# Performance work log

Measured on AMD Instinct MI355X. Metric: run time of the kernel, lower is better.

## Reference

```python
import jax, jax.numpy as jnp
import numpy as np

D_MODEL = 1024
NHEAD = 16
D_HEAD = D_MODEL // NHEAD
B, L = 2, 2048


def setup_inputs() -> dict:
    key = jax.random.key(0)
    ks = jax.random.split(key, 11)
    s = 1.0 / np.sqrt(D_MODEL)
    return {
        "Q": jax.random.normal(ks[0], (B, L, D_MODEL), jnp.float32),
        "K": jax.random.normal(ks[1], (B, L, D_MODEL), jnp.float32),
        "V": jax.random.normal(ks[2], (B, L, D_MODEL), jnp.float32),
        "Wq": jax.random.normal(ks[3], (D_MODEL, D_MODEL), jnp.float32) * s,
        "bq": jax.random.normal(ks[4], (D_MODEL,), jnp.float32) * 0.01,
        "Wk": jax.random.normal(ks[5], (D_MODEL, D_MODEL), jnp.float32) * s,
        "bk": jax.random.normal(ks[6], (D_MODEL,), jnp.float32) * 0.01,
        "Wv": jax.random.normal(ks[7], (D_MODEL, D_MODEL), jnp.float32) * s,
        "bv": jax.random.normal(ks[8], (D_MODEL,), jnp.float32) * 0.01,
        "Wo": jax.random.normal(ks[9], (D_MODEL, D_MODEL), jnp.float32) * s,
        "bo": jax.random.normal(ks[10], (D_MODEL,), jnp.float32) * 0.01,
    }


def reference(Q, K, V, Wq, bq, Wk, bk, Wv, bv, Wo, bo):
    b, l, _ = Q.shape
    # QKV linear projections (nn.Linear: x @ W.T + b), then split into heads
    q = (Q @ Wq.T + bq).reshape(b, l, NHEAD, D_HEAD)
    k = (K @ Wk.T + bk).reshape(b, l, NHEAD, D_HEAD)
    v = (V @ Wv.T + bv).reshape(b, l, NHEAD, D_HEAD)
    # scaled dot-product attention: softmax(QK^T / sqrt(d_head)) V
    scale = jnp.asarray(1.0 / np.sqrt(D_HEAD), q.dtype)
    scores = jnp.einsum("bqhd,bkhd->bhqk", q, k) * scale  # [B,H,L,L]
    attn = jax.nn.softmax(scores, axis=-1)
    out = jnp.einsum("bhqk,bkhd->bqhd", attn, v)  # [B,L,H,Dh]
    out = out.reshape(b, l, D_MODEL)  # concat heads
    return out @ Wo.T + bo
```

## Files before the change

kernel.cpp:

```cpp
#include <hip/hip_runtime.h>
#include <cstdint>
#include <cstddef>

#define DM 1024
#define NH 16
#define DH 64
#define NB 2
#define SQ 2048
#define MT (NB*SQ)

typedef float  f32x4  __attribute__((ext_vector_type(4)));
typedef float  f32x16 __attribute__((ext_vector_type(16)));
typedef short  s16x8 __attribute__((ext_vector_type(8)));
typedef short  s16x4 __attribute__((ext_vector_type(4)));

__device__ __forceinline__ unsigned short f2bf(float x) {
    unsigned int u = __float_as_uint(x);
    unsigned int lsb = (u >> 16) & 1u;
    u += 0x7fffu + lsb;
    return (unsigned short)(u >> 16);
}

__device__ __forceinline__ void gload16(const void* g, void* l) {
    __builtin_amdgcn_global_load_lds(
        (const __attribute__((address_space(1))) void*)g,
        (__attribute__((address_space(3))) void*)l,
        16, 0, 0);
}

__global__ __launch_bounds__(256) void castk(const float* __restrict__ in,
                                             unsigned short* __restrict__ out, int n) {
    int i = (blockIdx.x * 256 + threadIdx.x) * 4;
    if (i >= n) return;
    float4 a = *reinterpret_cast<const float4*>(in + i);
    s16x4 r;
    r[0] = (short)f2bf(a.x);
    r[1] = (short)f2bf(a.y);
    r[2] = (short)f2bf(a.z);
    r[3] = (short)f2bf(a.w);
    *reinterpret_cast<s16x4*>(out + i) = r;
}

__device__ __forceinline__ void gemm_core(const unsigned short* __restrict__ A,
                                          const unsigned short* __restrict__ Bm,
                                          int m0, int n0, int t,
                                          unsigned short (*As)[64],
                                          unsigned short (*Bs)[64],
                                          f32x4 acc[4][4]) {
    const int lane = t & 63, w = t >> 6;
    const int wm = (w >> 1) * 64, wn = (w & 1) * 64;
    const int lo = lane & 15, hi = lane >> 4;

    for (int k0 = 0; k0 < DM; k0 += 64) {
#pragma unroll
        for (int i = 0; i < 4; i++) {
            int c = i * 256 + t;
            int r = c >> 3, col = (c & 7) * 8;
            gload16(A  + (size_t)(m0 + r) * DM + k0 + col, &As[r][col]);
            gload16(Bm + (size_t)(n0 + r) * DM + k0 + col, &Bs[r][col]);
        }
        asm volatile("s_waitcnt vmcnt(0)" ::: "memory");
        __syncthreads();

#pragma unroll
        for (int kk = 0; kk < 64; kk += 32) {
            s16x8 a[4], b[4];
#pragma unroll
            for (int mi = 0; mi < 4; mi++)
                a[mi] = *reinterpret_cast<const s16x8*>(&As[wm + mi * 16 + lo][kk + hi * 8]);
#pragma unroll
            for (int ni = 0; ni < 4; ni++)
                b[ni] = *reinterpret_cast<const s16x8*>(&Bs[wn + ni * 16 + lo][kk + hi * 8]);
#pragma unroll
            for (int mi = 0; mi < 4; mi++)
#pragma unroll
                for (int ni = 0; ni < 4; ni++)
                    acc[mi][ni] = __builtin_amdgcn_mfma_f32_16x16x32_bf16(
                        a[mi], b[ni], acc[mi][ni], 0, 0, 0);
        }
        __syncthreads();
    }
}

__global__ __launch_bounds__(256, 3) void gemm_qkv(
    const unsigned short* __restrict__ Qb, const unsigned short* __restrict__ Kb,
    const unsigned short* __restrict__ Vb,
    const unsigned short* __restrict__ Wq, const unsigned short* __restrict__ Wk,
    const unsigned short* __restrict__ Wv,
    const float* __restrict__ bq, const float* __restrict__ bk, const float* __restrict__ bv,
    unsigned short* __restrict__ qp, unsigned short* __restrict__ kp,
    unsigned short* __restrict__ vt) {
    __shared__ __align__(16) unsigned short As[128][64];
    __shared__ __align__(16) unsigned short Bs[128][64];
    const int t = threadIdx.x;
    const int z = blockIdx.z;
    const unsigned short* A    = (z == 0) ? Qb : (z == 1) ? Kb : Vb;
    const unsigned short* Bm   = (z == 0) ? Wq : (z == 1) ? Wk : Wv;
    const float*          bias = (z == 0) ? bq : (z == 1) ? bk : bv;
    const int m0 = blockIdx.y * 128, n0 = blockIdx.x * 128;

    f32x4 acc[4][4] = {};
    gemm_core(A, Bm, m0, n0, t, As, Bs, acc);

    const int lane = t & 63, w = t >> 6;
    const int wm = (w >> 1) * 64, wn = (w & 1) * 64;
    const int lo = lane & 15, hi = lane >> 4;

    if (z < 2) {
        unsigned short* C = z ? kp : qp;
        const float scale = z ? 1.0f : 0.18033688011112042f;
#pragma unroll
        for (int mi = 0; mi < 4; mi++)
#pragma unroll
            for (int ni = 0; ni < 4; ni++) {
                int cc = n0 + wn + ni * 16 + lo;
                float bb = bias[cc];
#pragma unroll
                for (int j = 0; j < 4; j++) {
                    int rr = m0 + wm + mi * 16 + hi * 4 + j;
                    C[(size_t)rr * DM + cc] = f2bf((acc[mi][ni][j] + bb) * scale);
                }
            }
    } else {
#pragma unroll
        for (int mi = 0; mi < 4; mi++)
#pragma unroll
            for (int ni = 0; ni < 4; ni++) {
                int cc = n0 + wn + ni * 16 + lo;
                float bb = bias[cc];
#pragma unroll
                for (int j = 0; j < 4; j++) {
                    int rr = m0 + wm + mi * 16 + hi * 4 + j;
                    size_t idx = ((size_t)(rr >> 11) * DM + cc) * SQ + (rr & (SQ - 1));
                    vt[idx] = f2bf(acc[mi][ni][j] + bb);
                }
            }
    }
}

__global__ __launch_bounds__(256, 3) void gemm_out(
    const unsigned short* __restrict__ Ao, const unsigned short* __restrict__ Wo,
    const float* __restrict__ bo, float* __restrict__ Cout) {
    __shared__ __align__(16) unsigned short As[128][64];
    __shared__ __align__(16) unsigned short Bs[128][64];
    const int t = threadIdx.x;
    const int m0 = blockIdx.y * 128, n0 = blockIdx.x * 128;

    f32x4 acc[4][4] = {};
    gemm_core(Ao, Wo, m0, n0, t, As, Bs, acc);

    const int lane = t & 63, w = t >> 6;
    const int wm = (w >> 1) * 64, wn = (w & 1) * 64;
    const int lo = lane & 15, hi = lane >> 4;
#pragma unroll
    for (int mi = 0; mi < 4; mi++)
#pragma unroll
        for (int ni = 0; ni < 4; ni++) {
            int cc = n0 + wn + ni * 16 + lo;
            float bb = bo[cc];
#pragma unroll
            for (int j = 0; j < 4; j++) {
                int rr = m0 + wm + mi * 16 + hi * 4 + j;
                Cout[(size_t)rr * DM + cc] = acc[mi][ni][j] + bb;
            }
        }
}

__global__ __launch_bounds__(256, 2) void attn_k(
    const unsigned short* __restrict__ qp, const unsigned short* __restrict__ kp,
    const unsigned short* __restrict__ vt, unsigned short* __restrict__ ao) {
    __shared__ __align__(16) unsigned short Qs[128][64];
    __shared__ __align__(16) unsigned short Ks[128][64];
    __shared__ __align__(16) unsigned short Vs[64][128];

    const int t = threadIdx.x;
    const int lane = t & 63, w = t >> 6;
    const int l5 = lane & 31, hb = lane >> 5;
    const int q0 = blockIdx.x * 128;
    const int bh = blockIdx.y;
    const int b = bh >> 4, h = bh & 15;

#pragma unroll
    for (int i = 0; i < 4; i++) {
        int c = i * 256 + t;
        int r = c >> 3, col = ((c & 7) ^ (r & 7)) * 8;
        gload16(qp + (size_t)(b * SQ + q0 + r) * DM + h * DH + col, &Qs[r][(c & 7) * 8]);
    }

    float mrow = -1e30f, lrow = 0.0f;
    f32x16 oaccT[2] = {};
    s16x8 qfrag[4];

    for (int kt = 0; kt < SQ; kt += 128) {
#pragma unroll
        for (int i = 0; i < 4; i++) {
            int c = i * 256 + t;
            int r = c >> 3, col = ((c & 7) ^ (r & 7)) * 8;
            gload16(kp + (size_t)(b * SQ + kt + r) * DM + h * DH + col, &Ks[r][(c & 7) * 8]);
        }
#pragma unroll
        for (int i = 0; i < 4; i++) {
            int c = i * 256 + t;
            int r = c >> 4, col = ((c & 15) ^ (r & 15)) * 8;
            gload16(vt + (size_t)(bh * DH + r) * SQ + kt + col, &Vs[r][(c & 15) * 8]);
        }
        asm volatile("s_waitcnt vmcnt(0)" ::: "memory");
        __syncthreads();

        if (kt == 0) {
#pragma unroll
            for (int kk = 0; kk < 4; kk++) {
                int qr = w * 32 + l5;
                qfrag[kk] = *reinterpret_cast<const s16x8*>(
                    &Qs[qr][((kk * 2 + hb) ^ (qr & 7)) * 8]);
            }
        }

        f32x16 sT[4] = {};
#pragma unroll
        for (int ks = 0; ks < 4; ks++) {
#pragma unroll
            for (int kk = 0; kk < 4; kk++) {
                int kr = ks * 32 + l5;
                s16x8 kf = *reinterpret_cast<const s16x8*>(
                    &Ks[kr][((kk * 2 + hb) ^ (kr & 7)) * 8]);
                sT[ks] = __builtin_amdgcn_mfma_f32_32x32x16_bf16(
                    kf, qfrag[kk], sT[ks], 0, 0, 0);
            }
        }

        float mx = -3.0e38f;
#pragma unroll
        for (int ks = 0; ks < 4; ks++) {
            float a0 = fmaxf(fmaxf(sT[ks][0], sT[ks][1]), fmaxf(sT[ks][2], sT[ks][3]));
            float a1 = fmaxf(fmaxf(sT[ks][4], sT[ks][5]), fmaxf(sT[ks][6], sT[ks][7]));
            float a2 = fmaxf(fmaxf(sT[ks][8], sT[ks][9]), fmaxf(sT[ks][10], sT[ks][11]));
            float a3 = fmaxf(fmaxf(sT[ks][12], sT[ks][13]), fmaxf(sT[ks][14], sT[ks][15]));
            mx = fmaxf(mx, fmaxf(fmaxf(a0, a1), fmaxf(a2, a3)));
        }
        mx = fmaxf(mx, __shfl_xor(mx, 32));
        float mnew = fmaxf(mrow, mx);
        float fs = exp2f(mrow - mnew);
        mrow = mnew;
        float ps = 0.0f;
#pragma unroll
        for (int ks = 0; ks < 4; ks++)
#pragma unroll
            for (int r = 0; r < 16; r++) {
                float e = exp2f(sT[ks][r] - mnew);
                sT[ks][r] = e;
                ps += e;
            }
        ps += __shfl_xor(ps, 32);
        lrow = lrow * fs + ps;
        oaccT[0] *= fs;
        oaccT[1] *= fs;

#pragma unroll
        for (int ks = 0; ks < 4; ks++) {
            unsigned int pw0[4], pw1[4];
#pragma unroll
            for (int m = 0; m < 4; m++) {
                pw0[m] = (unsigned int)f2bf(sT[ks][4 * m]) |
                         ((unsigned int)f2bf(sT[ks][4 * m + 1]) << 16);
                pw1[m] = (unsigned int)f2bf(sT[ks][4 * m + 2]) |
                         ((unsigned int)f2bf(sT[ks][4 * m + 3]) << 16);
            }
#pragma unroll
            for (int tt = 0; tt < 2; tt++) {
                unsigned int s0 = hb ? pw0[2 * tt] : pw0[2 * tt + 1];
                unsigned int s1 = hb ? pw1[2 * tt] : pw1[2 * tt + 1];
                unsigned int r0 = __shfl_xor(s0, 32);
                unsigned int r1 = __shfl_xor(s1, 32);
                union { unsigned int u[4]; s16x8 v; } uu;
                if (hb == 0) { uu.u[0] = pw0[2 * tt]; uu.u[1] = pw1[2 * tt];
                               uu.u[2] = r0;          uu.u[3] = r1; }
                else         { uu.u[0] = r0;          uu.u[1] = r1;
                               uu.u[2] = pw0[2 * tt + 1]; uu.u[3] = pw1[2 * tt + 1]; }
                s16x8 pf = uu.v;
#pragma unroll
                for (int dblk = 0; dblk < 2; dblk++) {
                    int vr = dblk * 32 + l5;
                    int sl = ((ks * 2 + tt) * 2 + hb) ^ (vr & 15);
                    s16x8 vf = *reinterpret_cast<const s16x8*>(&Vs[vr][sl * 8]);
                    oaccT[dblk] = __builtin_amdgcn_mfma_f32_32x32x16_bf16(
                        vf, pf, oaccT[dblk], 0, 0, 0);
                }
            }
        }
        __syncthreads();
    }

    float inv = 1.0f / lrow;
    size_t rowbase = (size_t)(b * SQ + q0 + w * 32 + l5) * DM + h * DH;
#pragma unroll
    for (int dblk = 0; dblk < 2; dblk++)
#pragma unroll
        for (int g = 0; g < 4; g++) {
            s16x4 st;
#pragma unroll
            for (int j = 0; j < 4; j++)
                st[j] = (short)f2bf(oaccT[dblk][4 * g + j] * inv);
            *reinterpret_cast<s16x4*>(&ao[rowbase + dblk * 32 + 8 * g + 4 * hb]) = st;
        }
}

extern "C" void kernel_launch(void* const* d_in, const int* in_sizes, int n_in,
                              void* d_out, int out_size, void* d_ws, size_t ws_size,
                              hipStream_t stream) {
    const float* Q  = (const float*)d_in[0];
    const float* K  = (const float*)d_in[1];
    const float* V  = (const float*)d_in[2];
    const float* Wq = (const float*)d_in[3];
    const float* bq = (const float*)d_in[4];
    const float* Wk = (const float*)d_in[5];
    const float* bk = (const float*)d_in[6];
    const float* Wv = (const float*)d_in[7];
    const float* bv = (const float*)d_in[8];
    const float* Wo = (const float*)d_in[9];
    const float* bo = (const float*)d_in[10];

    char* ws = (char*)d_ws;
    size_t off = 0;
    auto alloc = [&](size_t bytes) {
        void* p = ws + off;
        off += (bytes + 255) & ~(size_t)255;
        return p;
    };
    const size_t XB = (size_t)MT * DM * 2;
    const size_t WB = (size_t)DM * DM * 2;
    unsigned short* qb  = (unsigned short*)alloc(XB);
    unsigned short* kb  = (unsigned short*)alloc(XB);
    unsigned short* vb  = (unsigned short*)alloc(XB);
    unsigned short* wqb = (unsigned short*)alloc(WB);
    unsigned short* wkb = (unsigned short*)alloc(WB);
    unsigned short* wvb = (unsigned short*)alloc(WB);
    unsigned short* wob = (unsigned short*)alloc(WB);
    unsigned short* qp  = (unsigned short*)alloc(XB);
    unsigned short* kp  = (unsigned short*)alloc(XB);
    unsigned short* vtp = (unsigned short*)alloc(XB);
    unsigned short* ao  = (unsigned short*)alloc(XB);

    castk<<<dim3(MT * DM / 1024), 256, 0, stream>>>(Q, qb, MT * DM);
    castk<<<dim3(MT * DM / 1024), 256, 0, stream>>>(K, kb, MT * DM);
    castk<<<dim3(MT * DM / 1024), 256, 0, stream>>>(V, vb, MT * DM);
    castk<<<dim3(DM * DM / 1024), 256, 0, stream>>>(Wq, wqb, DM * DM);
    castk<<<dim3(DM * DM / 1024), 256, 0, stream>>>(Wk, wkb, DM * DM);
    castk<<<dim3(DM * DM / 1024), 256, 0, stream>>>(Wv, wvb, DM * DM);
    castk<<<dim3(DM * DM / 1024), 256, 0, stream>>>(Wo, wob, DM * DM);

    gemm_qkv<<<dim3(DM / 128, MT / 128, 3), 256, 0, stream>>>(
        qb, kb, vb, wqb, wkb, wvb, bq, bk, bv, qp, kp, vtp);

    attn_k<<<dim3(SQ / 128, NB * NH), 256, 0, stream>>>(qp, kp, vtp, ao);

    gemm_out<<<dim3(DM / 128, MT / 128), 256, 0, stream>>>(ao, wob, bo, (float*)d_out);
}
```

Measured before the change: 269.2 us.

## Tune attention softmax: lazy rescale, packed bf16 converts, direct Q loads, setprio

Several changes to the attention kernel. Q fragments are loaded straight from global memory into registers, which drops the Q shared-memory tile. The online-softmax rescale is skipped unless the max grows by more than a threshold, and the reductions use fewer dependent ops. Manual bf16 rounding is replaced with the hardware v_cvt_pk_bf16_f32 instruction, and MFMA sections are wrapped in s_setprio. The V-transpose store in the projection GEMM is also vectorised to 4-element writes. Together these aim to cut VALU work in softmax and free LDS. The lazy rescale lets unnormalised exponentials reach up to 2^8, which risks some precision.

```diff
diff --git a/kernel.cpp b/kernel.cpp
--- a/kernel.cpp
+++ b/kernel.cpp
@@ -19,6 +19,12 @@
     unsigned int lsb = (u >> 16) & 1u;
     u += 0x7fffu + lsb;
     return (unsigned short)(u >> 16);
+}
+
+__device__ __forceinline__ unsigned int cvtpk(float lo, float hi) {
+    unsigned int r;
+    asm("v_cvt_pk_bf16_f32 %0, %1, %2" : "=v"(r) : "v"(lo), "v"(hi));
+    return r;
 }
 
 __device__ __forceinline__ void gload16(const void* g, void* l) {
@@ -128,12 +134,13 @@
             for (int ni = 0; ni < 4; ni++) {
                 int cc = n0 + wn + ni * 16 + lo;
                 float bb = bias[cc];
-#pragma unroll
-                for (int j = 0; j < 4; j++) {
-                    int rr = m0 + wm + mi * 16 + hi * 4 + j;
-                    size_t idx = ((size_t)(rr >> 11) * DM + cc) * SQ + (rr & (SQ - 1));
-                    vt[idx] = f2bf(acc[mi][ni][j] + bb);
-                }
+                int rr0 = m0 + wm + mi * 16 + hi * 4;
+                size_t base = ((size_t)(rr0 >> 11) * DM + cc) * SQ + (rr0 & (SQ - 1));
+                s16x4 st;
+#pragma unroll
+                for (int j = 0; j < 4; j++)
+                    st[j] = (short)f2bf(acc[mi][ni][j] + bb);
+                *reinterpret_cast<s16x4*>(&vt[base]) = st;
             }
     }
 }
@@ -169,7 +176,6 @@
 __global__ __launch_bounds__(256, 2) void attn_k(
     const unsigned short* __restrict__ qp, const unsigned short* __restrict__ kp,
     const unsigned short* __restrict__ vt, unsigned short* __restrict__ ao) {
-    __shared__ __align__(16) unsigned short Qs[128][64];
     __shared__ __align__(16) unsigned short Ks[128][64];
     __shared__ __align__(16) unsigned short Vs[64][128];
 
@@ -180,16 +186,14 @@
     const int bh = blockIdx.y;
     const int b = bh >> 4, h = bh & 15;
 
-#pragma unroll
-    for (int i = 0; i < 4; i++) {
-        int c = i * 256 + t;
-        int r = c >> 3, col = ((c & 7) ^ (r & 7)) * 8;
-        gload16(qp + (size_t)(b * SQ + q0 + r) * DM + h * DH + col, &Qs[r][(c & 7) * 8]);
-    }
+    const unsigned short* qrow = qp + (size_t)(b * SQ + q0 + w * 32 + l5) * DM + h * DH;
+    s16x8 qfrag[4];
+#pragma unroll
+    for (int kk = 0; kk < 4; kk++)
+        qfrag[kk] = *reinterpret_cast<const s16x8*>(qrow + kk * 16 + hb * 8);
 
     float mrow = -1e30f, lrow = 0.0f;
     f32x16 oaccT[2] = {};
-    s16x8 qfrag[4];
 
     for (int kt = 0; kt < SQ; kt += 128) {
 #pragma unroll
@@ -207,16 +211,8 @@
         asm volatile("s_waitcnt vmcnt(0)" ::: "memory");
         __syncthreads();
 
-        if (kt == 0) {
-#pragma unroll
-            for (int kk = 0; kk < 4; kk++) {
-                int qr = w * 32 + l5;
-                qfrag[kk] = *reinterpret_cast<const s16x8*>(
-                    &Qs[qr][((kk * 2 + hb) ^ (qr & 7)) * 8]);
-            }
-        }
-
         f32x16 sT[4] = {};
+        __builtin_amdgcn_s_setprio(1);
 #pragma unroll
         for (int ks = 0; ks < 4; ks++) {
 #pragma unroll
@@ -228,43 +224,55 @@
                     kf, qfrag[kk], sT[ks], 0, 0, 0);
             }
         }
+        __builtin_amdgcn_s_setprio(0);
 
         float mx = -3.0e38f;
 #pragma unroll
         for (int ks = 0; ks < 4; ks++) {
-            float a0 = fmaxf(fmaxf(sT[ks][0], sT[ks][1]), fmaxf(sT[ks][2], sT[ks][3]));
-            float a1 = fmaxf(fmaxf(sT[ks][4], sT[ks][5]), fmaxf(sT[ks][6], sT[ks][7]));
-            float a2 = fmaxf(fmaxf(sT[ks][8], sT[ks][9]), fmaxf(sT[ks][10], sT[ks][11]));
-            float a3 = fmaxf(fmaxf(sT[ks][12], sT[ks][13]), fmaxf(sT[ks][14], sT[ks][15]));
-            mx = fmaxf(mx, fmaxf(fmaxf(a0, a1), fmaxf(a2, a3)));
+            float t0 = fmaxf(fmaxf(sT[ks][0], sT[ks][1]), sT[ks][2]);
+            float t1 = fmaxf(fmaxf(sT[ks][3], sT[ks][4]), sT[ks][5]);
+            float t2 = fmaxf(fmaxf(sT[ks][6], sT[ks][7]), sT[ks][8]);
+            float t3 = fmaxf(fmaxf(sT[ks][9], sT[ks][10]), sT[ks][11]);
+            float t4 = fmaxf(fmaxf(sT[ks][12], sT[ks][13]), sT[ks][14]);
+            float t5 = fmaxf(fmaxf(sT[ks][15], t0), t1);
+            float t6 = fmaxf(fmaxf(t2, t3), t4);
+            mx = fmaxf(fmaxf(mx, t5), t6);
         }
         mx = fmaxf(mx, __shfl_xor(mx, 32));
-        float mnew = fmaxf(mrow, mx);
-        float fs = exp2f(mrow - mnew);
-        mrow = mnew;
-        float ps = 0.0f;
+
+        if (!__all(mx <= mrow + 8.0f)) {
+            float mnew = fmaxf(mrow, mx);
+            float fs = exp2f(mrow - mnew);
+            mrow = mnew;
+            lrow *= fs;
+            oaccT[0] *= fs;
+            oaccT[1] *= fs;
+        }
+
+        float ps0 = 0.0f, ps1 = 0.0f, ps2 = 0.0f, ps3 = 0.0f;
 #pragma unroll
         for (int ks = 0; ks < 4; ks++)
 #pragma unroll
-            for (int r = 0; r < 16; r++) {
-                float e = exp2f(sT[ks][r] - mnew);
-                sT[ks][r] = e;
-                ps += e;
-            }
+            for (int r = 0; r < 16; r += 4) {
+                float e0 = exp2f(sT[ks][r]     - mrow);
+                float e1 = exp2f(sT[ks][r + 1] - mrow);
+                float e2 = exp2f(sT[ks][r + 2] - mrow);
+                float e3 = exp2f(sT[ks][r + 3] - mrow);
+                sT[ks][r] = e0; sT[ks][r + 1] = e1;
+                sT[ks][r + 2] = e2; sT[ks][r + 3] = e3;
+                ps0 += e0; ps1 += e1; ps2 += e2; ps3 += e3;
+            }
+        float ps = (ps0 + ps1) + (ps2 + ps3);
         ps += __shfl_xor(ps, 32);
-        lrow = lrow * fs + ps;
-        oaccT[0] *= fs;
-        oaccT[1] *= fs;
+        lrow += ps;
 
 #pragma unroll
         for (int ks = 0; ks < 4; ks++) {
             unsigned int pw0[4], pw1[4];
 #pragma unroll
             for (int m = 0; m < 4; m++) {
-                pw0[m] = (unsigned int)f2bf(sT[ks][4 * m]) |
-                         ((unsigned int)f2bf(sT[ks][4 * m + 1]) << 16);
-                pw1[m] = (unsigned int)f2bf(sT[ks][4 * m + 2]) |
-                         ((unsigned int)f2bf(sT[ks][4 * m + 3]) << 16);
+                pw0[m] = cvtpk(sT[ks][4 * m], sT[ks][4 * m + 1]);
+                pw1[m] = cvtpk(sT[ks][4 * m + 2], sT[ks][4 * m + 3]);
             }
 #pragma unroll
             for (int tt = 0; tt < 2; tt++) {
@@ -278,6 +286,7 @@
                 else         { uu.u[0] = r0;          uu.u[1] = r1;
                                uu.u[2] = pw0[2 * tt + 1]; uu.u[3] = pw1[2 * tt + 1]; }
                 s16x8 pf = uu.v;
+                __builtin_amdgcn_s_setprio(1);
 #pragma unroll
                 for (int dblk = 0; dblk < 2; dblk++) {
                     int vr = dblk * 32 + l5;
@@ -286,6 +295,7 @@
                     oaccT[dblk] = __builtin_amdgcn_mfma_f32_32x32x16_bf16(
                         vf, pf, oaccT[dblk], 0, 0, 0);
                 }
+                __builtin_amdgcn_s_setprio(0);
             }
         }
         __syncthreads();
@@ -297,11 +307,10 @@
     for (int dblk = 0; dblk < 2; dblk++)
 #pragma unroll
         for (int g = 0; g < 4; g++) {
-            s16x4 st;
-#pragma unroll
-            for (int j = 0; j < 4; j++)
-                st[j] = (short)f2bf(oaccT[dblk][4 * g + j] * inv);
-            *reinterpret_cast<s16x4*>(&ao[rowbase + dblk * 32 + 8 * g + 4 * hb]) = st;
+            unsigned int w0 = cvtpk(oaccT[dblk][4 * g] * inv, oaccT[dblk][4 * g + 1] * inv);
+            unsigned int w1 = cvtpk(oaccT[dblk][4 * g + 2] * inv, oaccT[dblk][4 * g + 3] * inv);
+            uint2 st = make_uint2(w0, w1);
+            *reinterpret_cast<uint2*>(&ao[rowbase + dblk * 32 + 8 * g + 4 * hb]) = st;
         }
 }
 
```

New measurement: 263.0 us. 2.3% less time.
